# Performance work log

Hardware: AMD Instinct MI355X
Metric: run time of the kernel (lower is better)

The kernel has to match this reference:

```python
import jax, jax.numpy as jnp
import numpy as np

N_NODES = 102400
N_FEAT = 128
N_TPLT = 16
N_TPLT_NODES = 10
N_GRAPHS = 256
EPS = 1.0       # entropic regularization for the Sinkhorn OT solve
N_ITER = 50     # fixed Sinkhorn iterations


def setup_inputs() -> dict:
    key = jax.random.key(0)
    k1, k2 = jax.random.split(key)
    x = jax.random.normal(k1, (N_NODES, N_FEAT), dtype=jnp.float32)
    # template features ~ N(feature_init_mean=0, feature_init_std=1)
    tplt_features = jax.random.normal(k2, (N_TPLT, N_TPLT_NODES, N_FEAT), dtype=jnp.float32)
    # q0 initialized so softmax(q0) is uniform over template nodes
    q0 = jnp.zeros((N_TPLT, N_TPLT_NODES), dtype=jnp.float32)
    # equal-size graphs: 400 nodes per graph, sorted batch vector (PyG convention)
    batch = jnp.repeat(jnp.arange(N_GRAPHS, dtype=jnp.int32), N_NODES // N_GRAPHS)
    return {"x": x, "tplt_features": tplt_features, "q0": q0,
            "batch": batch, "num_graphs": N_GRAPHS}


def _wasserstein_to_templates(x, tplt_features, q0, batch, num_graphs):
    # x: [N, d] node features; tplt_features: [K, M, d]; q0: [K, M]; batch: [N]
    N = x.shape[0]
    K, M, d = tplt_features.shape
    # squared-Euclidean cost C[n,k,m] = ||x_n - T_km||^2   (ot.dist default)
    C = (jnp.sum(x * x, axis=-1)[:, None, None]
         + jnp.sum(tplt_features * tplt_features, axis=-1)[None, :, :]
         - 2.0 * jnp.einsum('nd,kmd->nkm', x, tplt_features))  # [N,K,M]

    # uniform node weights per graph: a_n = 1/|S_{batch[n]}|
    counts = jax.ops.segment_sum(jnp.ones((N,), x.dtype), batch, num_segments=num_graphs)
    log_a = -jnp.log(counts)[batch]                      # [N]
    # template node weights b = softmax(q0, axis=1)
    log_b = jax.nn.log_softmax(q0, axis=1)               # [K,M]

    def seg_lse(t):  # logsumexp over nodes within each graph; t: [N,K,M] -> [G,K,M]
        m = jax.ops.segment_max(t, batch, num_segments=num_graphs)
        s = jax.ops.segment_sum(jnp.exp(t - m[batch]), batch, num_segments=num_graphs)
        return m + jnp.log(s)

    def f_update(g):  # [G,K,M] -> [N,K]
        return EPS * (log_a[:, None] - jax.nn.logsumexp((g[batch] - C) / EPS, axis=2))

    def step(g, _):
        f = f_update(g)
        g_new = EPS * (log_b[None, :, :] - seg_lse((f[:, :, None] - C) / EPS))
        return g_new, None

    g0 = jnp.zeros((num_graphs, K, M), x.dtype)
    g, _ = jax.lax.scan(step, g0, None, length=N_ITER)
    f = f_update(g)
    # transport plan P[n,k,m] = exp((f + g - C)/eps); OT cost = <P, C> per (graph, template)
    logP = (f[:, :, None] + g[batch] - C) / EPS          # [N,K,M]
    per_node = jnp.sum(jnp.exp(logP) * C, axis=2)        # [N,K]
    return jax.ops.segment_sum(per_node, batch, num_segments=num_graphs)  # [G,K]


def reference(x, tplt_features, q0, batch, num_graphs):
    return _wasserstein_to_templates(x, tplt_features, q0, batch, num_graphs)
```

## Files before the change

### kernel.cpp

```cpp
#include <hip/hip_runtime.h>

#define K_TPLT 16
#define M_NODES 10
#define DFEAT 128
#define NMAX 7
#define N_ITER 50
#define NEG_BIG -1e30f
#define LOG2E 1.44269504088896340736f
#define LN2   0.69314718055994530942f

#define EXP2F(x) __builtin_amdgcn_exp2f(x)
#define LOG2F(x) __builtin_amdgcn_logf(x)

__global__ void zero_counts_k(int* counts, int G) {
    int g = blockIdx.x * blockDim.x + threadIdx.x;
    if (g < G) counts[g] = 0;
}

__global__ void count_nodes_k(const int* __restrict__ batch, int* counts, int N) {
    int i = blockIdx.x * blockDim.x + threadIdx.x;
    if (i < N) atomicAdd(&counts[batch[i]], 1);
}

__global__ void scan_counts_k(const int* __restrict__ counts, int* starts, int G) {
    __shared__ int sc[1024];
    int t = threadIdx.x;
    for (int g = t; g < G; g += blockDim.x) sc[g] = counts[g];
    __syncthreads();
    for (int g = t; g < G; g += blockDim.x) {
        int s = 0;
        for (int j = 0; j < g; ++j) s += sc[j];
        starts[g] = s;
    }
}

template <int CTRL>
__device__ __forceinline__ float dpp_add(float v) {
    return v + __int_as_float(__builtin_amdgcn_update_dpp(
        0, __float_as_int(v), CTRL, 0xF, 0xF, true));
}
__device__ __forceinline__ float wred_add(float v) {
    v = dpp_add<0xB1>(v);
    v = dpp_add<0x4E>(v);
    v = dpp_add<0x141>(v);
    v = dpp_add<0x140>(v);
    v += __shfl_xor(v, 16);
    v += __shfl_xor(v, 32);
    return v;
}
template <int CTRL>
__device__ __forceinline__ float dpp_max(float v) {
    return fmaxf(v, __int_as_float(__builtin_amdgcn_update_dpp(
        0, __float_as_int(v), CTRL, 0xF, 0xF, true)));
}
__device__ __forceinline__ float wred_max(float v) {
    v = dpp_max<0xB1>(v);
    v = dpp_max<0x4E>(v);
    v = dpp_max<0x141>(v);
    v = dpp_max<0x140>(v);
    v = fmaxf(v, __shfl_xor(v, 16));
    v = fmaxf(v, __shfl_xor(v, 32));
    return v;
}

__global__ __launch_bounds__(64) void sinkhorn_tw_k(
    const float* __restrict__ x, const float* __restrict__ tplt,
    const float* __restrict__ q0, const int* __restrict__ starts,
    const int* __restrict__ counts, float* __restrict__ out, int G)
{
    const int bid  = blockIdx.x;
    const int g    = bid % G;
    const int k    = bid / G;
    const int lane = threadIdx.x;

    const int start = starts[g];
    const int count = counts[g];
    const float a   = 1.0f / (float)count;
    const float la2 = -LOG2F((float)count);

    const float* qk = q0 + k * M_NODES;
    float lbla[M_NODES];
    {
        float qv[M_NODES];
        float qmax = NEG_BIG;
#pragma unroll
        for (int m = 0; m < M_NODES; ++m) { qv[m] = qk[m]; qmax = fmaxf(qmax, qv[m]); }
        float qs = 0.f;
#pragma unroll
        for (int m = 0; m < M_NODES; ++m) {
            qv[m] = (qv[m] - qmax) * LOG2E;
            qs += EXP2F(qv[m]);
        }
        const float corr = LOG2F(qs);
#pragma unroll
        for (int m = 0; m < M_NODES; ++m) lbla[m] = qv[m] - corr - la2;
    }

    bool act[NMAX];
#pragma unroll
    for (int i = 0; i < NMAX; ++i) act[i] = (lane + i * 64) < count;

    float L[NMAX][M_NODES];
    float nsh[NMAX];
    float csh[M_NODES];
    {
        const float* Tk = tplt + (size_t)k * M_NODES * DFEAT;
        float x2[NMAX];
        float t2[M_NODES];
#pragma unroll
        for (int i = 0; i < NMAX; ++i) {
            x2[i] = 0.f;
#pragma unroll
            for (int m = 0; m < M_NODES; ++m) L[i][m] = 0.f;
        }
#pragma unroll
        for (int m = 0; m < M_NODES; ++m) t2[m] = 0.f;

        for (int j = 0; j < DFEAT; j += 4) {
            float4 xv[NMAX];
#pragma unroll
            for (int i = 0; i < NMAX; ++i) {
                if (act[i]) {
                    xv[i] = *(const float4*)(x + (size_t)(start + lane + i * 64) * DFEAT + j);
                } else {
                    xv[i].x = xv[i].y = xv[i].z = xv[i].w = 0.f;
                }
                x2[i] += xv[i].x * xv[i].x + xv[i].y * xv[i].y
                       + xv[i].z * xv[i].z + xv[i].w * xv[i].w;
            }
#pragma unroll
            for (int m = 0; m < M_NODES; ++m) {
                const float4 tv = *(const float4*)(Tk + m * DFEAT + j);
                t2[m] += tv.x * tv.x + tv.y * tv.y + tv.z * tv.z + tv.w * tv.w;
#pragma unroll
                for (int i = 0; i < NMAX; ++i) {
                    L[i][m] += xv[i].x * tv.x + xv[i].y * tv.y
                             + xv[i].z * tv.z + xv[i].w * tv.w;
                }
            }
        }
#pragma unroll
        for (int i = 0; i < NMAX; ++i) {
            float mx = NEG_BIG;
#pragma unroll
            for (int m = 0; m < M_NODES; ++m) {
                L[i][m] = (2.f * L[i][m] - x2[i] - t2[m]) * LOG2E;
                mx = fmaxf(mx, L[i][m]);
            }
            nsh[i] = mx;
#pragma unroll
            for (int m = 0; m < M_NODES; ++m) L[i][m] -= mx;
        }
#pragma unroll
        for (int m = 0; m < M_NODES; ++m) {
            float c = NEG_BIG;
#pragma unroll
            for (int i = 0; i < NMAX; ++i) c = act[i] ? fmaxf(c, L[i][m]) : c;
            csh[m] = wred_max(c);
        }
    }

    float g2[M_NODES];

    {
        float w0[M_NODES], acc[M_NODES];
#pragma unroll
        for (int m = 0; m < M_NODES; ++m) { w0[m] = EXP2F(csh[m]); acc[m] = 0.f; }
#pragma unroll
        for (int i = 0; i < NMAX; ++i) {
            if (act[i]) {
                float E[M_NODES];
                float D = 0.f;
#pragma unroll
                for (int m = 0; m < M_NODES; ++m) {
                    E[m] = EXP2F(L[i][m] - csh[m]);
                    D = fmaf(E[m], w0[m], D);
                }
                const float r = __builtin_amdgcn_rcpf(D);
#pragma unroll
                for (int m = 0; m < M_NODES; ++m) acc[m] = fmaf(E[m], r, acc[m]);
            }
        }
#pragma unroll
        for (int m = 0; m < M_NODES; ++m) {
            const float s = wred_add(acc[m]);
            g2[m] = lbla[m] - csh[m] - LOG2F(fmaxf(s, 1e-35f));
        }
    }

    for (int it = 1; it < N_ITER; ++it) {
        float acc[M_NODES];
#pragma unroll
        for (int m = 0; m < M_NODES; ++m) acc[m] = 0.f;

#pragma unroll
        for (int i = 0; i < NMAX; ++i) {
            if (act[i]) {
                float e[M_NODES];
                float zmax = NEG_BIG;
#pragma unroll
                for (int m = 0; m < M_NODES; ++m) {
                    e[m] = g2[m] + L[i][m];
                    zmax = fmaxf(zmax, e[m]);
                }
                float D = 0.f;
#pragma unroll
                for (int m = 0; m < M_NODES; ++m) { e[m] = EXP2F(e[m] - zmax); D += e[m]; }
                const float r = __builtin_amdgcn_rcpf(D);
#pragma unroll
                for (int m = 0; m < M_NODES; ++m) acc[m] = fmaf(e[m], r, acc[m]);
            }
        }
#pragma unroll
        for (int m = 0; m < M_NODES; ++m) {
            const float s = wred_add(acc[m]);
            g2[m] = lbla[m] + g2[m] - LOG2F(fmaxf(s, 1e-35f));
        }
    }

    float accum = 0.f;
#pragma unroll
    for (int i = 0; i < NMAX; ++i) {
        if (act[i]) {
            float e[M_NODES];
            float zmax = NEG_BIG;
#pragma unroll
            for (int m = 0; m < M_NODES; ++m) {
                e[m] = g2[m] + L[i][m];
                zmax = fmaxf(zmax, e[m]);
            }
            float D = 0.f;
#pragma unroll
            for (int m = 0; m < M_NODES; ++m) { e[m] = EXP2F(e[m] - zmax); D += e[m]; }
            const float r = __builtin_amdgcn_rcpf(D);
            float q = 0.f;
#pragma unroll
            for (int m = 0; m < M_NODES; ++m) q = fmaf(e[m], L[i][m], q);
            accum += nsh[i] + q * r;
        }
    }
    accum = wred_add(accum);
    if (lane == 0) out[(size_t)g * K_TPLT + k] = -a * LN2 * accum;
}

extern "C" void kernel_launch(void* const* d_in, const int* in_sizes, int n_in,
                              void* d_out, int out_size, void* d_ws, size_t ws_size,
                              hipStream_t stream) {
    const float* x    = (const float*)d_in[0];
    const float* tplt = (const float*)d_in[1];
    const float* q0   = (const float*)d_in[2];
    const int* batch  = (const int*)d_in[3];
    const int N = in_sizes[3];
    const int G = out_size / K_TPLT;

    int* counts = (int*)d_ws;
    int* starts = counts + G;

    zero_counts_k<<<(G + 255) / 256, 256, 0, stream>>>(counts, G);
    count_nodes_k<<<(N + 255) / 256, 256, 0, stream>>>(batch, counts, N);
    scan_counts_k<<<1, 256, 0, stream>>>(counts, starts, G);
    sinkhorn_tw_k<<<G * K_TPLT, 64, 0, stream>>>(x, tplt, q0, starts, counts,
                                                 (float*)d_out, G);
}
```

Before: 518.4 us.

## Process two templates per wavefront to share x loads and add ILP

Each 64-thread block now handles two template problems (k0 and k0+8) for the same graph, so the grid is halved. The x rows are loaded once and dotted against both templates, and the Sinkhorn loop interleaves two independent problems to hide exp/reduction latency. The cost is doubled register state (L grows to 2x7x10 floats), which risks lower occupancy or spills, plus fewer blocks in flight.

```diff
diff --git a/kernel.cpp b/kernel.cpp
--- a/kernel.cpp
+++ b/kernel.cpp
@@ -4,6 +4,7 @@
 #define M_NODES 10
 #define DFEAT 128
 #define NMAX 7
+#define NPROB 2
 #define N_ITER 50
 #define NEG_BIG -1e30f
 #define LOG2E 1.44269504088896340736f
@@ -70,7 +71,7 @@
 {
     const int bid  = blockIdx.x;
     const int g    = bid % G;
-    const int k    = bid / G;
+    const int k0   = bid / G;
     const int lane = threadIdx.x;
 
     const int start = starts[g];
@@ -78,9 +79,10 @@
     const float a   = 1.0f / (float)count;
     const float la2 = -LOG2F((float)count);
 
-    const float* qk = q0 + k * M_NODES;
-    float lbla[M_NODES];
-    {
+    float lbla[NPROB][M_NODES];
+#pragma unroll
+    for (int p = 0; p < NPROB; ++p) {
+        const float* qk = q0 + (k0 + 8 * p) * M_NODES;
         float qv[M_NODES];
         float qmax = NEG_BIG;
 #pragma unroll
@@ -93,28 +95,33 @@
         }
         const float corr = LOG2F(qs);
 #pragma unroll
-        for (int m = 0; m < M_NODES; ++m) lbla[m] = qv[m] - corr - la2;
+        for (int m = 0; m < M_NODES; ++m) lbla[p][m] = qv[m] - corr - la2;
     }
 
     bool act[NMAX];
 #pragma unroll
     for (int i = 0; i < NMAX; ++i) act[i] = (lane + i * 64) < count;
 
-    float L[NMAX][M_NODES];
-    float nsh[NMAX];
-    float csh[M_NODES];
+    float L[NPROB][NMAX][M_NODES];
+    float nsum[NPROB];
+    float csh[NPROB][M_NODES];
     {
-        const float* Tk = tplt + (size_t)k * M_NODES * DFEAT;
+        const float* Tk0 = tplt + (size_t)k0 * M_NODES * DFEAT;
+        const float* Tk1 = tplt + (size_t)(k0 + 8) * M_NODES * DFEAT;
         float x2[NMAX];
-        float t2[M_NODES];
+        float t2[NPROB][M_NODES];
 #pragma unroll
         for (int i = 0; i < NMAX; ++i) {
             x2[i] = 0.f;
 #pragma unroll
-            for (int m = 0; m < M_NODES; ++m) L[i][m] = 0.f;
-        }
-#pragma unroll
-        for (int m = 0; m < M_NODES; ++m) t2[m] = 0.f;
+            for (int p = 0; p < NPROB; ++p)
+#pragma unroll
+                for (int m = 0; m < M_NODES; ++m) L[p][i][m] = 0.f;
+        }
+#pragma unroll
+        for (int p = 0; p < NPROB; ++p)
+#pragma unroll
+            for (int m = 0; m < M_NODES; ++m) t2[p][m] = 0.f;
 
         for (int j = 0; j < DFEAT; j += 4) {
             float4 xv[NMAX];
@@ -130,42 +137,51 @@
             }
 #pragma unroll
             for (int m = 0; m < M_NODES; ++m) {
-                const float4 tv = *(const float4*)(Tk + m * DFEAT + j);
-                t2[m] += tv.x * tv.x + tv.y * tv.y + tv.z * tv.z + tv.w * tv.w;
+                const float4 tv0 = *(const float4*)(Tk0 + m * DFEAT + j);
+                const float4 tv1 = *(const float4*)(Tk1 + m * DFEAT + j);
+                t2[0][m] += tv0.x * tv0.x + tv0.y * tv0.y + tv0.z * tv0.z + tv0.w * tv0.w;
+                t2[1][m] += tv1.x * tv1.x + tv1.y * tv1.y + tv1.z * tv1.z + tv1.w * tv1.w;
 #pragma unroll
                 for (int i = 0; i < NMAX; ++i) {
-                    L[i][m] += xv[i].x * tv.x + xv[i].y * tv.y
-                             + xv[i].z * tv.z + xv[i].w * tv.w;
-                }
-            }
-        }
-#pragma unroll
-        for (int i = 0; i < NMAX; ++i) {
-            float mx = NEG_BIG;
+                    L[0][i][m] += xv[i].x * tv0.x + xv[i].y * tv0.y
+                                + xv[i].z * tv0.z + xv[i].w * tv0.w;
+                    L[1][i][m] += xv[i].x * tv1.x + xv[i].y * tv1.y
+                                + xv[i].z * tv1.z + xv[i].w * tv1.w;
+                }
+            }
+        }
+#pragma unroll
+        for (int p = 0; p < NPROB; ++p) {
+            nsum[p] = 0.f;
+#pragma unroll
+            for (int i = 0; i < NMAX; ++i) {
+                float mx = NEG_BIG;
+#pragma unroll
+                for (int m = 0; m < M_NODES; ++m) {
+                    L[p][i][m] = (2.f * L[p][i][m] - x2[i] - t2[p][m]) * LOG2E;
+                    mx = fmaxf(mx, L[p][i][m]);
+                }
+                if (act[i]) nsum[p] += mx;
+#pragma unroll
+                for (int m = 0; m < M_NODES; ++m) L[p][i][m] -= mx;
+            }
 #pragma unroll
             for (int m = 0; m < M_NODES; ++m) {
-                L[i][m] = (2.f * L[i][m] - x2[i] - t2[m]) * LOG2E;
-                mx = fmaxf(mx, L[i][m]);
-            }
-            nsh[i] = mx;
-#pragma unroll
-            for (int m = 0; m < M_NODES; ++m) L[i][m] -= mx;
-        }
-#pragma unroll
-        for (int m = 0; m < M_NODES; ++m) {
-            float c = NEG_BIG;
-#pragma unroll
-            for (int i = 0; i < NMAX; ++i) c = act[i] ? fmaxf(c, L[i][m]) : c;
-            csh[m] = wred_max(c);
-        }
-    }
-
-    float g2[M_NODES];
-
-    {
+                float c = NEG_BIG;
+#pragma unroll
+                for (int i = 0; i < NMAX; ++i) c = act[i] ? fmaxf(c, L[p][i][m]) : c;
+                csh[p][m] = wred_max(c);
+            }
+        }
+    }
+
+    float g2[NPROB][M_NODES];
+
+#pragma unroll
+    for (int p = 0; p < NPROB; ++p) {
         float w0[M_NODES], acc[M_NODES];
 #pragma unroll
-        for (int m = 0; m < M_NODES; ++m) { w0[m] = EXP2F(csh[m]); acc[m] = 0.f; }
+        for (int m = 0; m < M_NODES; ++m) { w0[m] = EXP2F(csh[p][m]); acc[m] = 0.f; }
 #pragma unroll
         for (int i = 0; i < NMAX; ++i) {
             if (act[i]) {
@@ -173,7 +189,7 @@
                 float D = 0.f;
 #pragma unroll
                 for (int m = 0; m < M_NODES; ++m) {
-                    E[m] = EXP2F(L[i][m] - csh[m]);
+                    E[m] = EXP2F(L[p][i][m] - csh[p][m]);
                     D = fmaf(E[m], w0[m], D);
                 }
                 const float r = __builtin_amdgcn_rcpf(D);
@@ -184,15 +200,50 @@
 #pragma unroll
         for (int m = 0; m < M_NODES; ++m) {
             const float s = wred_add(acc[m]);
-            g2[m] = lbla[m] - csh[m] - LOG2F(fmaxf(s, 1e-35f));
+            g2[p][m] = lbla[p][m] - csh[p][m] - LOG2F(fmaxf(s, 1e-35f));
         }
     }
 
     for (int it = 1; it < N_ITER; ++it) {
-        float acc[M_NODES];
-#pragma unroll
-        for (int m = 0; m < M_NODES; ++m) acc[m] = 0.f;
-
+        float acc[NPROB][M_NODES];
+#pragma unroll
+        for (int p = 0; p < NPROB; ++p)
+#pragma unroll
+            for (int m = 0; m < M_NODES; ++m) acc[p][m] = 0.f;
+
+#pragma unroll
+        for (int i = 0; i < NMAX; ++i) {
+            if (act[i]) {
+#pragma unroll
+                for (int p = 0; p < NPROB; ++p) {
+                    float e[M_NODES];
+                    float zmax = NEG_BIG;
+#pragma unroll
+                    for (int m = 0; m < M_NODES; ++m) {
+                        e[m] = g2[p][m] + L[p][i][m];
+                        zmax = fmaxf(zmax, e[m]);
+                    }
+                    float D = 0.f;
+#pragma unroll
+                    for (int m = 0; m < M_NODES; ++m) { e[m] = EXP2F(e[m] - zmax); D += e[m]; }
+                    const float r = __builtin_amdgcn_rcpf(D);
+#pragma unroll
+                    for (int m = 0; m < M_NODES; ++m) acc[p][m] = fmaf(e[m], r, acc[p][m]);
+                }
+            }
+        }
+#pragma unroll
+        for (int p = 0; p < NPROB; ++p)
+#pragma unroll
+            for (int m = 0; m < M_NODES; ++m) {
+                const float s = wred_add(acc[p][m]);
+                g2[p][m] = lbla[p][m] + g2[p][m] - LOG2F(fmaxf(s, 1e-35f));
+            }
+    }
+
+#pragma unroll
+    for (int p = 0; p < NPROB; ++p) {
+        float accum = nsum[p];
 #pragma unroll
         for (int i = 0; i < NMAX; ++i) {
             if (act[i]) {
@@ -200,47 +251,22 @@
                 float zmax = NEG_BIG;
 #pragma unroll
                 for (int m = 0; m < M_NODES; ++m) {
-                    e[m] = g2[m] + L[i][m];
+                    e[m] = g2[p][m] + L[p][i][m];
                     zmax = fmaxf(zmax, e[m]);
                 }
                 float D = 0.f;
 #pragma unroll
                 for (int m = 0; m < M_NODES; ++m) { e[m] = EXP2F(e[m] - zmax); D += e[m]; }
                 const float r = __builtin_amdgcn_rcpf(D);
-#pragma unroll
-                for (int m = 0; m < M_NODES; ++m) acc[m] = fmaf(e[m], r, acc[m]);
-            }
-        }
-#pragma unroll
-        for (int m = 0; m < M_NODES; ++m) {
-            const float s = wred_add(acc[m]);
-            g2[m] = lbla[m] + g2[m] - LOG2F(fmaxf(s, 1e-35f));
-        }
-    }
-
-    float accum = 0.f;
-#pragma unroll
-    for (int i = 0; i < NMAX; ++i) {
-        if (act[i]) {
-            float e[M_NODES];
-            float zmax = NEG_BIG;
-#pragma unroll
-            for (int m = 0; m < M_NODES; ++m) {
-                e[m] = g2[m] + L[i][m];
-                zmax = fmaxf(zmax, e[m]);
-            }
-            float D = 0.f;
-#pragma unroll
-            for (int m = 0; m < M_NODES; ++m) { e[m] = EXP2F(e[m] - zmax); D += e[m]; }
-            const float r = __builtin_amdgcn_rcpf(D);
-            float q = 0.f;
-#pragma unroll
-            for (int m = 0; m < M_NODES; ++m) q = fmaf(e[m], L[i][m], q);
-            accum += nsh[i] + q * r;
-        }
-    }
-    accum = wred_add(accum);
-    if (lane == 0) out[(size_t)g * K_TPLT + k] = -a * LN2 * accum;
+                float q = 0.f;
+#pragma unroll
+                for (int m = 0; m < M_NODES; ++m) q = fmaf(e[m], L[p][i][m], q);
+                accum += q * r;
+            }
+        }
+        accum = wred_add(accum);
+        if (lane == 0) out[(size_t)g * K_TPLT + (k0 + 8 * p)] = -a * LN2 * accum;
+    }
 }
 
 extern "C" void kernel_launch(void* const* d_in, const int* in_sizes, int n_in,
@@ -259,6 +285,6 @@
     zero_counts_k<<<(G + 255) / 256, 256, 0, stream>>>(counts, G);
     count_nodes_k<<<(N + 255) / 256, 256, 0, stream>>>(batch, counts, N);
     scan_counts_k<<<1, 256, 0, stream>>>(counts, starts, G);
-    sinkhorn_tw_k<<<G * K_TPLT, 64, 0, stream>>>(x, tplt, q0, starts, counts,
-                                                 (float*)d_out, G);
-}
+    sinkhorn_tw_k<<<G * (K_TPLT / 2), 64, 0, stream>>>(x, tplt, q0, starts, counts,
+                                                       (float*)d_out, G);
+}
```

Measured after the change: 486.2 us. -6.2%, faster.
